# Performance work log

Hardware: AMD Instinct MI355X
Metric: run time of the kernel (lower is better)

The kernel has to match this reference:

```python
import jax, jax.numpy as jnp
import numpy as np

LN_EPS = 1e-5


def setup_inputs() -> dict:
    key = jax.random.key(0)
    ks = jax.random.split(key, 6)
    B, N, C, H = 8, 4096, 768, 12
    D = C // H
    x = jax.random.normal(ks[0], (B, N, C), dtype=jnp.float32)
    w_qkv = jax.random.normal(ks[1], (3 * C, C), dtype=jnp.float32) * (C ** -0.5)
    w_proj = jax.random.normal(ks[2], (C, C), dtype=jnp.float32) * (C ** -0.5)
    b_proj = jnp.zeros((C,), dtype=jnp.float32)
    # trunc_normal_(std=0.02) approximated by clipped normal
    p1 = jnp.clip(jax.random.normal(ks[3], (H, N), dtype=jnp.float32) * 0.02, -0.04, 0.04)
    p2 = jnp.clip(jax.random.normal(ks[4], (H, N), dtype=jnp.float32) * 0.02, -0.04, 0.04)
    gamma = jnp.ones((D,), dtype=jnp.float32)
    beta = jnp.zeros((D,), dtype=jnp.float32)
    return {"x": x, "w_qkv": w_qkv, "w_proj": w_proj, "b_proj": b_proj,
            "p1": p1, "p2": p2, "gamma": gamma, "beta": beta}


def _layernorm(h, gamma, beta):
    mu = jnp.mean(h, axis=-1, keepdims=True)
    var = jnp.var(h, axis=-1, keepdims=True)
    return (h - mu) * jax.lax.rsqrt(var + LN_EPS) * gamma + beta


def reference(x, w_qkv, w_proj, b_proj, p1, p2, gamma, beta):
    B, N, C = x.shape
    H = p1.shape[0]
    D = C // H
    # qkv projection (no bias): [B,N,3C] -> [3,B,H,N,D]
    qkv = (x @ w_qkv.T).reshape(B, N, 3, H, D).transpose(2, 0, 3, 1, 4)
    q, k, v = qkv[0], qkv[1], qkv[2]
    # weighted k*v reduction over sequence: [B,H,D]
    modulator = jnp.einsum('hn,bhnd->bhd', p2, k * v)
    modulator = _layernorm(modulator, gamma, beta)
    # broadcast modulation back over N: [B,H,N,D]
    modulator = jnp.einsum('hn,bhd->bhnd', p1, modulator)
    out = (q * modulator).transpose(0, 2, 1, 3).reshape(B, N, C)
    return out @ w_proj.T + b_proj
```

## Files before the change

kernel.cpp:

```cpp
#include <hip/hip_runtime.h>
#include <stdint.h>
#include <stddef.h>

#define LN_EPS 1e-5f

typedef __bf16 bf16;
typedef __bf16 bf16x8 __attribute__((ext_vector_type(8)));
typedef __bf16 bf16x4 __attribute__((ext_vector_type(4)));
typedef float f32x4 __attribute__((ext_vector_type(4)));

#define GL16(gp, lp)                                                                   \
  __builtin_amdgcn_global_load_lds((__attribute__((address_space(1))) uint32_t*)(gp),  \
                                   (__attribute__((address_space(3))) uint32_t*)(lp),  \
                                   16, 0, 0)

#define SBAR   asm volatile("s_barrier" ::: "memory")
#define LGK0   asm volatile("s_waitcnt lgkmcnt(0)" ::: "memory")
#define VMW(N) asm volatile("s_waitcnt vmcnt(" #N ")" ::: "memory")
#define NOWAIT ((void)0)

#define XV4   6291456
#define WQV4  442368
#define WPV4  147456
__global__ __launch_bounds__(256) void cvt_all(const float* __restrict__ x,
                                               const float* __restrict__ wq,
                                               const float* __restrict__ wp,
                                               bf16* __restrict__ xb,
                                               bf16* __restrict__ wqb,
                                               bf16* __restrict__ wpb) {
  int i = blockIdx.x * 256 + threadIdx.x;
  const float* src; bf16* dst; int off;
  if (i < XV4)              { src = x;  dst = xb;  off = i; }
  else if (i < XV4 + WQV4)  { src = wq; dst = wqb; off = i - XV4; }
  else                      { src = wp; dst = wpb; off = i - (XV4 + WQV4); }
  const float4 v = ((const float4*)src)[off];
  bf16x4 o;
  o[0] = (bf16)v.x; o[1] = (bf16)v.y; o[2] = (bf16)v.z; o[3] = (bf16)v.w;
  ((bf16x4*)dst)[off] = o;
}

#define STAGE_A(T, KH, SLOT) do {                      \
    GL16(pA0 + (T)*64 + (KH)*32, dA + (SLOT)*8192);    \
    GL16(pA1 + (T)*64 + (KH)*32, dA + (SLOT)*8192 + 4096); } while (0)

#define STAGE_B(T, KH, SLOT) do {                      \
    GL16(pB0 + (T)*64 + (KH)*32, dB + (SLOT)*8192);    \
    GL16(pB1 + (T)*64 + (KH)*32, dB + (SLOT)*8192 + 4096); } while (0)

#define PHASE(SLOT, MH, RB, STG, WAIT) do {                                         \
    if (RB) {                                                                       \
      _Pragma("unroll") for (int n = 0; n < 4; ++n)                                 \
        bF[n] = *(const bf16x8*)(ldsB + (SLOT)*8192 + (rB + n*16)*32 + colE);       \
    }                                                                               \
    _Pragma("unroll") for (int m = 0; m < 4; ++m)                                   \
      aF[m] = *(const bf16x8*)(ldsA + (SLOT)*8192 + (rA + (MH)*64 + m*16)*32 + colE); \
    STG;                                                                            \
    SBAR;                                                                           \
    LGK0;                                                                           \
    __builtin_amdgcn_sched_barrier(0);                                              \
    __builtin_amdgcn_s_setprio(1);                                                  \
    _Pragma("unroll") for (int m = 0; m < 4; ++m)                                   \
      _Pragma("unroll") for (int n = 0; n < 4; ++n)                                 \
        acc[(MH)*4 + m][n] =                                                        \
            __builtin_amdgcn_mfma_f32_16x16x32_bf16(aF[m], bF[n],                   \
                                                    acc[(MH)*4 + m][n], 0, 0, 0);   \
    __builtin_amdgcn_s_setprio(0);                                                  \
    WAIT;                                                                           \
    SBAR;                                                                           \
  } while (0)

#define TILE(SB, ST1, ST2, ST3, ST4, W2, W4) do { \
    PHASE((SB),     0, true,  ST1, NOWAIT);       \
    PHASE((SB),     1, false, ST2, W2);           \
    PHASE((SB) + 1, 0, true,  ST3, NOWAIT);       \
    PHASE((SB) + 1, 1, false, ST4, W4);           \
  } while (0)

__device__ __forceinline__ void gemm256(const bf16* pA0, const bf16* pA1,
                                        const bf16* pB0, const bf16* pB1,
                                        bf16* sh, f32x4 acc[8][4]) {
  const int tid  = threadIdx.x;
  const int lane = tid & 63;
  const int wave = tid >> 6;
  const int wm   = wave >> 2;
  const int wn   = wave & 3;
  const int l16  = lane & 15;
  const int colE = ((((lane >> 4) * 16) ^ (((l16 >> 1) & 3) << 4)) >> 1);
  bf16* const ldsA = sh;
  bf16* const ldsB = sh + 32768;
  bf16* const dA   = ldsA + tid * 8;
  bf16* const dB   = ldsB + tid * 8;
  const int rA = wm * 128 + l16;
  const int rB = wn * 64 + l16;
  bf16x8 aF[4], bF[4];

  STAGE_A(0, 0, 0); STAGE_B(0, 0, 0);
  STAGE_A(0, 1, 1); STAGE_B(0, 1, 1);
  STAGE_A(1, 0, 2); STAGE_B(1, 0, 2);
  VMW(8);
  SBAR;

  for (int T = 0; T < 10; T += 2) {
    TILE(0, STAGE_A(T+1,1,3), STAGE_B(T+1,1,3), STAGE_A(T+2,0,0), STAGE_B(T+2,0,0), VMW(8), VMW(8));
    TILE(2, STAGE_A(T+2,1,1), STAGE_B(T+2,1,1), STAGE_A(T+3,0,2), STAGE_B(T+3,0,2), VMW(8), VMW(8));
  }
  TILE(0, STAGE_A(11,1,3), STAGE_B(11,1,3), NOWAIT, NOWAIT, VMW(8), VMW(4));
  TILE(2, NOWAIT, NOWAIT, NOWAIT, NOWAIT, VMW(0), NOWAIT);

  asm volatile("s_waitcnt vmcnt(0) lgkmcnt(0)" ::: "memory");
  __syncthreads();
}

__global__ __launch_bounds__(512, 2) void kv_gemm_reduce(const bf16* __restrict__ A,
                                                         const bf16* __restrict__ B,
                                                         const float* __restrict__ p2,
                                                         float* __restrict__ partials) {
  __shared__ __align__(16) bf16 sh[65536];
  __shared__ float red[4][2][64];

  int lin = blockIdx.y * 6 + blockIdx.x;
  lin = (lin & 7) * 96 + (lin >> 3);
  const int hh   = lin % 6;
  const int mblk = lin / 6;
  const int m0   = mblk * 256;
  const int h0   = hh * 2;

  const int tid = threadIdx.x;
  const int rr  = tid >> 2;
  const int ck  = ((tid & 3) ^ ((tid >> 3) & 3)) * 8;
  const bf16* pA0 = A + (size_t)(m0 + rr) * 768 + ck;
  const bf16* pA1 = pA0 + (size_t)128 * 768;
  const int r1 = 128 + rr;
  const int wr0 = 768 + (((rr >> 6) & 1) * 768) + (h0 + (rr >> 7)) * 64 + (rr & 63);
  const int wr1 = 768 + (((r1 >> 6) & 1) * 768) + (h0 + (r1 >> 7)) * 64 + (r1 & 63);
  const bf16* pB0 = B + (size_t)wr0 * 768 + ck;
  const bf16* pB1 = B + (size_t)wr1 * 768 + ck;

  f32x4 acc[8][4] = {};
  gemm256(pA0, pA1, pB0, pB1, sh, acc);

  const int lane = tid & 63, wave = tid >> 6;
  const int wm = wave >> 2, wn = wave & 3, l16 = lane & 15;
  const int crow0 = wm * 128 + (lane >> 4) * 4;
  const int ccol0 = wn * 64 + l16;
#pragma unroll
  for (int mi = 0; mi < 8; ++mi)
#pragma unroll
    for (int ni = 0; ni < 4; ++ni)
#pragma unroll
      for (int r = 0; r < 4; ++r) {
        const int row = crow0 + mi * 16 + r;
        const int col = ccol0 + ni * 16;
        sh[row * 256 + (col ^ (((row >> 2) & 3) << 4))] = (bf16)acc[mi][ni][r];
      }
  __syncthreads();

  const int chunk = tid >> 7, hl = (tid >> 6) & 1, d = tid & 63;
  const float* pw = p2 + (size_t)(h0 + hl) * 4096 + (m0 & 4095) + chunk * 64;
  float s = 0.f;
#pragma unroll 8
  for (int n = 0; n < 64; ++n) {
    const int row = chunk * 64 + n;
    const int x = ((row >> 2) & 3) << 4;
    const float kk = (float)sh[row * 256 + ((hl * 128 + d) ^ x)];
    const float vv = (float)sh[row * 256 + ((hl * 128 + 64 + d) ^ x)];
    s += pw[n] * kk * vv;
  }
  red[chunk][hl][d] = s;
  __syncthreads();
  if (tid < 128) {
    const int hx = tid >> 6, dd = tid & 63;
    partials[((size_t)mblk * 12 + h0 + hx) * 64 + dd] =
        red[0][hx][dd] + red[1][hx][dd] + red[2][hx][dd] + red[3][hx][dd];
  }
}

__global__ __launch_bounds__(64) void mod_reduce_ln(const float* __restrict__ partials,
                                                    const float* __restrict__ gamma,
                                                    const float* __restrict__ beta,
                                                    float* __restrict__ mod) {
  const int h = blockIdx.x, b = blockIdx.y;
  const int d = threadIdx.x;

  const float* p = partials + ((size_t)(b * 16) * 12 + h) * 64 + d;
  float s = 0.f;
#pragma unroll
  for (int mb = 0; mb < 16; ++mb) s += p[(size_t)mb * 12 * 64];

  float sum = s, sumsq = s * s;
#pragma unroll
  for (int o = 32; o > 0; o >>= 1) {
    sum   += __shfl_xor(sum, o);
    sumsq += __shfl_xor(sumsq, o);
  }
  const float mu  = sum * (1.f / 64.f);
  const float var = sumsq * (1.f / 64.f) - mu * mu;
  const float r   = rsqrtf(var + LN_EPS);
  mod[(b * 12 + h) * 64 + d] = (s - mu) * r * gamma[d] + beta[d];
}

__global__ __launch_bounds__(512, 2) void q_gemm_mod(const bf16* __restrict__ A,
                                                     const bf16* __restrict__ B,
                                                     const float* __restrict__ p1,
                                                     const float* __restrict__ mod,
                                                     bf16* __restrict__ amod) {
  __shared__ __align__(16) bf16 sh[65536];

  int lin = blockIdx.y * 3 + blockIdx.x;
  lin = (lin & 7) * 48 + (lin >> 3);
  const int n0 = (lin % 3) * 256;
  const int m0 = (lin / 3) * 256;

  const int tid = threadIdx.x;
  const int rr  = tid >> 2;
  const int ck  = ((tid & 3) ^ ((tid >> 3) & 3)) * 8;
  const bf16* pA0 = A + (size_t)(m0 + rr) * 768 + ck;
  const bf16* pA1 = pA0 + (size_t)128 * 768;
  const bf16* pB0 = B + (size_t)(n0 + rr) * 768 + ck;
  const bf16* pB1 = pB0 + (size_t)128 * 768;

  f32x4 acc[8][4] = {};
  gemm256(pA0, pA1, pB0, pB1, sh, acc);

  const int lane = tid & 63, wave = tid >> 6;
  const int wm = wave >> 2, wn = wave & 3, l16 = lane & 15;
  const int row0 = m0 + wm * 128 + (lane >> 4) * 4;
  const int col0 = n0 + wn * 64 + l16;
  const int b    = m0 >> 12;
  const int h    = (n0 >> 6) + wn;

  float p1v[8][4];
#pragma unroll
  for (int mi = 0; mi < 8; ++mi)
#pragma unroll
    for (int r = 0; r < 4; ++r)
      p1v[mi][r] = p1[(size_t)h * 4096 + ((row0 + mi * 16 + r) & 4095)];
  float mv[4];
#pragma unroll
  for (int ni = 0; ni < 4; ++ni) mv[ni] = mod[b * 768 + col0 + ni * 16];

#pragma unroll
  for (int mi = 0; mi < 8; ++mi)
#pragma unroll
    for (int ni = 0; ni < 4; ++ni)
#pragma unroll
      for (int r = 0; r < 4; ++r)
        amod[(size_t)(row0 + mi * 16 + r) * 768 + col0 + ni * 16] =
            (bf16)(acc[mi][ni][r] * p1v[mi][r] * mv[ni]);
}

__global__ __launch_bounds__(512, 2) void gemm_proj(const bf16* __restrict__ A,
                                                    const bf16* __restrict__ B,
                                                    const float* __restrict__ bias,
                                                    float* __restrict__ C) {
  __shared__ __align__(16) bf16 sh[65536];

  int lin = blockIdx.y * 3 + blockIdx.x;
  lin = (lin & 7) * 48 + (lin >> 3);
  const int n0 = (lin % 3) * 256;
  const int m0 = (lin / 3) * 256;

  const int tid = threadIdx.x;
  const int rr  = tid >> 2;
  const int ck  = ((tid & 3) ^ ((tid >> 3) & 3)) * 8;
  const bf16* pA0 = A + (size_t)(m0 + rr) * 768 + ck;
  const bf16* pA1 = pA0 + (size_t)128 * 768;
  const bf16* pB0 = B + (size_t)(n0 + rr) * 768 + ck;
  const bf16* pB1 = pB0 + (size_t)128 * 768;

  f32x4 acc[8][4] = {};
  gemm256(pA0, pA1, pB0, pB1, sh, acc);

  const int lane = tid & 63, wave = tid >> 6;
  const int wm = wave >> 2, wn = wave & 3, l16 = lane & 15;
  const int row0 = m0 + wm * 128 + (lane >> 4) * 4;
  const int col0 = n0 + wn * 64 + l16;
#pragma unroll
  for (int ni = 0; ni < 4; ++ni) {
    const int col = col0 + ni * 16;
    const float bv = bias[col];
#pragma unroll
    for (int mi = 0; mi < 8; ++mi)
#pragma unroll
      for (int r = 0; r < 4; ++r)
        C[(size_t)(row0 + mi * 16 + r) * 768 + col] = acc[mi][ni][r] + bv;
  }
}

extern "C" void kernel_launch(void* const* d_in, const int* in_sizes, int n_in,
                              void* d_out, int out_size, void* d_ws, size_t ws_size,
                              hipStream_t stream) {
  (void)in_sizes; (void)n_in; (void)out_size; (void)ws_size;

  const float* x      = (const float*)d_in[0];
  const float* w_qkv  = (const float*)d_in[1];
  const float* w_proj = (const float*)d_in[2];
  const float* b_proj = (const float*)d_in[3];
  const float* p1     = (const float*)d_in[4];
  const float* p2     = (const float*)d_in[5];
  const float* gamma  = (const float*)d_in[6];
  const float* beta   = (const float*)d_in[7];
  float* out = (float*)d_out;

  char* ws = (char*)d_ws;
  bf16*  xb       = (bf16*)(ws + 0);
  bf16*  wqb      = (bf16*)(ws + 50331648);
  bf16*  wpb      = (bf16*)(ws + 53870592);
  bf16*  amod     = (bf16*)(ws + 55050240);
  float* partials = (float*)(ws + 105381888);
  float* mod      = (float*)(ws + 106168320);

  cvt_all<<<26880, 256, 0, stream>>>(x, w_qkv, w_proj, xb, wqb, wpb);

  kv_gemm_reduce<<<dim3(6, 128), 512, 0, stream>>>(xb, wqb, p2, partials);

  mod_reduce_ln<<<dim3(12, 8), 64, 0, stream>>>(partials, gamma, beta, mod);

  q_gemm_mod<<<dim3(3, 128), 512, 0, stream>>>(xb, wqb, p1, mod, amod);

  gemm_proj<<<dim3(3, 128), 512, 0, stream>>>(amod, wpb, b_proj, out);
}
```

Before: 379.5 us.

## Double-buffer LDS fragment reads across phases and transpose epilogue staging layout

Restructures the GEMM main loop so the A/B fragment reads for the next phase are issued before the MFMAs of the current phase. Two register sets of fragments alternate, and partial lgkmcnt waits replace the full wait, which removes one barrier per phase and overlaps LDS reads with matrix math. The k*v epilogue now writes accumulators transposed into a padded (264-wide) LDS tile with packed 4-element stores. The reduction then reads 8-element vectors along the sequence instead of scalar swizzled loads. This costs more registers and a slightly larger LDS footprint, which could hurt occupancy at 2 blocks per CU.

```diff
diff --git a/kernel.cpp b/kernel.cpp
--- a/kernel.cpp
+++ b/kernel.cpp
@@ -15,8 +15,8 @@
                                    16, 0, 0)
 
 #define SBAR   asm volatile("s_barrier" ::: "memory")
-#define LGK0   asm volatile("s_waitcnt lgkmcnt(0)" ::: "memory")
 #define VMW(N) asm volatile("s_waitcnt vmcnt(" #N ")" ::: "memory")
+#define LGK(N) asm volatile("s_waitcnt lgkmcnt(" #N ")" ::: "memory")
 #define NOWAIT ((void)0)
 
 #define XV4   6291456
@@ -39,41 +39,54 @@
   ((bf16x4*)dst)[off] = o;
 }
 
-#define STAGE_A(T, KH, SLOT) do {                      \
-    GL16(pA0 + (T)*64 + (KH)*32, dA + (SLOT)*8192);    \
-    GL16(pA1 + (T)*64 + (KH)*32, dA + (SLOT)*8192 + 4096); } while (0)
-
-#define STAGE_B(T, KH, SLOT) do {                      \
-    GL16(pB0 + (T)*64 + (KH)*32, dB + (SLOT)*8192);    \
-    GL16(pB1 + (T)*64 + (KH)*32, dB + (SLOT)*8192 + 4096); } while (0)
-
-#define PHASE(SLOT, MH, RB, STG, WAIT) do {                                         \
-    if (RB) {                                                                       \
-      _Pragma("unroll") for (int n = 0; n < 4; ++n)                                 \
-        bF[n] = *(const bf16x8*)(ldsB + (SLOT)*8192 + (rB + n*16)*32 + colE);       \
-    }                                                                               \
-    _Pragma("unroll") for (int m = 0; m < 4; ++m)                                   \
-      aF[m] = *(const bf16x8*)(ldsA + (SLOT)*8192 + (rA + (MH)*64 + m*16)*32 + colE); \
-    STG;                                                                            \
-    SBAR;                                                                           \
-    LGK0;                                                                           \
-    __builtin_amdgcn_sched_barrier(0);                                              \
-    __builtin_amdgcn_s_setprio(1);                                                  \
-    _Pragma("unroll") for (int m = 0; m < 4; ++m)                                   \
-      _Pragma("unroll") for (int n = 0; n < 4; ++n)                                 \
-        acc[(MH)*4 + m][n] =                                                        \
-            __builtin_amdgcn_mfma_f32_16x16x32_bf16(aF[m], bF[n],                   \
-                                                    acc[(MH)*4 + m][n], 0, 0, 0);   \
-    __builtin_amdgcn_s_setprio(0);                                                  \
-    WAIT;                                                                           \
-    SBAR;                                                                           \
+#define STAGE_A2(H, SL) do {                          \
+    GL16(pA0 + (H)*32, dA + (SL)*8192);               \
+    GL16(pA1 + (H)*32, dA + (SL)*8192 + 4096); } while (0)
+
+#define STAGE_B2(H, SL) do {                          \
+    GL16(pB0 + (H)*32, dB + (SL)*8192);               \
+    GL16(pB1 + (H)*32, dB + (SL)*8192 + 4096); } while (0)
+
+#define RD_B(DST, SL)                                                              \
+    _Pragma("unroll") for (int n = 0; n < 4; ++n)                                  \
+      DST[n] = *(const bf16x8*)(ldsB + (SL)*8192 + (rB + n*16)*32 + colE)
+
+#define RD_A0(DST, SL)                                                             \
+    _Pragma("unroll") for (int m = 0; m < 4; ++m)                                  \
+      DST[m] = *(const bf16x8*)(ldsA + (SL)*8192 + (rA + m*16)*32 + colE)
+
+#define RD_A1(SL)                                                                  \
+    _Pragma("unroll") for (int m = 0; m < 4; ++m)                                  \
+      af1[m] = *(const bf16x8*)(ldsA + (SL)*8192 + (rA + 64 + m*16)*32 + colE)
+
+#define MM(AF, BF, MO)                                                             \
+    _Pragma("unroll") for (int m = 0; m < 4; ++m)                                  \
+      _Pragma("unroll") for (int n = 0; n < 4; ++n)                                \
+        acc[(MO) + m][n] = __builtin_amdgcn_mfma_f32_16x16x32_bf16(                \
+            AF[m], BF[n], acc[(MO) + m][n], 0, 0, 0)
+
+#define EV_PHASE(SL, A0C, BFC, STG, WAITV) do {       \
+    RD_A1(SL);                                        \
+    STG;                                              \
+    LGK(4);                                           \
+    __builtin_amdgcn_sched_barrier(0);                \
+    __builtin_amdgcn_s_setprio(1);                    \
+    MM(A0C, BFC, 0);                                  \
+    __builtin_amdgcn_s_setprio(0);                    \
+    WAITV;                                            \
+    SBAR;                                             \
   } while (0)
 
-#define TILE(SB, ST1, ST2, ST3, ST4, W2, W4) do { \
-    PHASE((SB),     0, true,  ST1, NOWAIT);       \
-    PHASE((SB),     1, false, ST2, W2);           \
-    PHASE((SB) + 1, 0, true,  ST3, NOWAIT);       \
-    PHASE((SB) + 1, 1, false, ST4, W4);           \
+#define OD_PHASE(NSL, A0N, BFN, BFC, STG, LGKW) do {  \
+    RD_B(BFN, NSL);                                   \
+    RD_A0(A0N, NSL);                                  \
+    STG;                                              \
+    LGKW;                                             \
+    __builtin_amdgcn_sched_barrier(0);                \
+    __builtin_amdgcn_s_setprio(1);                    \
+    MM(af1, BFC, 4);                                  \
+    __builtin_amdgcn_s_setprio(0);                    \
+    SBAR;                                             \
   } while (0)
 
 __device__ __forceinline__ void gemm256(const bf16* pA0, const bf16* pA1,
@@ -92,21 +105,38 @@
   bf16* const dB   = ldsB + tid * 8;
   const int rA = wm * 128 + l16;
   const int rB = wn * 64 + l16;
-  bf16x8 aF[4], bF[4];
-
-  STAGE_A(0, 0, 0); STAGE_B(0, 0, 0);
-  STAGE_A(0, 1, 1); STAGE_B(0, 1, 1);
-  STAGE_A(1, 0, 2); STAGE_B(1, 0, 2);
+  bf16x8 af0X[4], af0Y[4], af1[4], bfX[4], bfY[4];
+
+  STAGE_A2(0, 0); STAGE_B2(0, 0);
+  STAGE_A2(1, 1); STAGE_B2(1, 1);
+  STAGE_A2(2, 2); STAGE_B2(2, 2);
   VMW(8);
   SBAR;
-
-  for (int T = 0; T < 10; T += 2) {
-    TILE(0, STAGE_A(T+1,1,3), STAGE_B(T+1,1,3), STAGE_A(T+2,0,0), STAGE_B(T+2,0,0), VMW(8), VMW(8));
-    TILE(2, STAGE_A(T+2,1,1), STAGE_B(T+2,1,1), STAGE_A(T+3,0,2), STAGE_B(T+3,0,2), VMW(8), VMW(8));
-  }
-  TILE(0, STAGE_A(11,1,3), STAGE_B(11,1,3), NOWAIT, NOWAIT, VMW(8), VMW(4));
-  TILE(2, NOWAIT, NOWAIT, NOWAIT, NOWAIT, VMW(0), NOWAIT);
-
+  RD_B(bfX, 0);
+  RD_A0(af0X, 0);
+
+  for (int h4 = 0; h4 < 20; h4 += 4) {
+    EV_PHASE(0, af0X, bfX, STAGE_A2(h4 + 3, 3), VMW(6));
+    OD_PHASE(1, af0Y, bfY, bfX, STAGE_B2(h4 + 3, 3), LGK(8));
+    EV_PHASE(1, af0Y, bfY, STAGE_A2(h4 + 4, 0), VMW(6));
+    OD_PHASE(2, af0X, bfX, bfY, STAGE_B2(h4 + 4, 0), LGK(8));
+    EV_PHASE(2, af0X, bfX, STAGE_A2(h4 + 5, 1), VMW(6));
+    OD_PHASE(3, af0Y, bfY, bfX, STAGE_B2(h4 + 5, 1), LGK(8));
+    EV_PHASE(3, af0Y, bfY, STAGE_A2(h4 + 6, 2), VMW(6));
+    OD_PHASE(0, af0X, bfX, bfY, STAGE_B2(h4 + 6, 2), LGK(8));
+  }
+  EV_PHASE(0, af0X, bfX, STAGE_A2(23, 3), VMW(6));
+  OD_PHASE(1, af0Y, bfY, bfX, STAGE_B2(23, 3), LGK(8));
+  EV_PHASE(1, af0Y, bfY, NOWAIT, VMW(4));
+  OD_PHASE(2, af0X, bfX, bfY, NOWAIT, LGK(8));
+  EV_PHASE(2, af0X, bfX, NOWAIT, VMW(0));
+  OD_PHASE(3, af0Y, bfY, bfX, NOWAIT, LGK(8));
+  EV_PHASE(3, af0Y, bfY, NOWAIT, NOWAIT);
+  LGK(0);
+  __builtin_amdgcn_sched_barrier(0);
+  __builtin_amdgcn_s_setprio(1);
+  MM(af1, bfY, 4);
+  __builtin_amdgcn_s_setprio(0);
   asm volatile("s_waitcnt vmcnt(0) lgkmcnt(0)" ::: "memory");
   __syncthreads();
 }
@@ -115,7 +145,7 @@
                                                          const bf16* __restrict__ B,
                                                          const float* __restrict__ p2,
                                                          float* __restrict__ partials) {
-  __shared__ __align__(16) bf16 sh[65536];
+  __shared__ __align__(16) bf16 sh[256 * 264];
   __shared__ float red[4][2][64];
 
   int lin = blockIdx.y * 6 + blockIdx.x;
@@ -141,32 +171,33 @@
 
   const int lane = tid & 63, wave = tid >> 6;
   const int wm = wave >> 2, wn = wave & 3, l16 = lane & 15;
-  const int crow0 = wm * 128 + (lane >> 4) * 4;
-  const int ccol0 = wn * 64 + l16;
-#pragma unroll
-  for (int mi = 0; mi < 8; ++mi)
-#pragma unroll
-    for (int ni = 0; ni < 4; ++ni)
-#pragma unroll
-      for (int r = 0; r < 4; ++r) {
-        const int row = crow0 + mi * 16 + r;
-        const int col = ccol0 + ni * 16;
-        sh[row * 256 + (col ^ (((row >> 2) & 3) << 4))] = (bf16)acc[mi][ni][r];
-      }
+  const int c0 = wn * 64 + l16;
+  const int r0 = wm * 128 + (lane >> 4) * 4;
+#pragma unroll
+  for (int ni = 0; ni < 4; ++ni)
+#pragma unroll
+    for (int mi = 0; mi < 8; ++mi) {
+      bf16x4 pk;
+      pk[0] = (bf16)acc[mi][ni][0]; pk[1] = (bf16)acc[mi][ni][1];
+      pk[2] = (bf16)acc[mi][ni][2]; pk[3] = (bf16)acc[mi][ni][3];
+      *(bf16x4*)(sh + (size_t)(c0 + ni * 16) * 264 + r0 + mi * 16) = pk;
+    }
   __syncthreads();
 
-  const int chunk = tid >> 7, hl = (tid >> 6) & 1, d = tid & 63;
-  const float* pw = p2 + (size_t)(h0 + hl) * 4096 + (m0 & 4095) + chunk * 64;
+  const int nq = tid >> 7, hl = (tid >> 6) & 1, d = tid & 63;
+  const float* pw = p2 + (size_t)(h0 + hl) * 4096 + (m0 & 4095) + nq * 64;
+  const bf16* pk = sh + (size_t)(hl * 128 + d) * 264 + nq * 64;
+  const bf16* pv = sh + (size_t)(hl * 128 + 64 + d) * 264 + nq * 64;
   float s = 0.f;
-#pragma unroll 8
-  for (int n = 0; n < 64; ++n) {
-    const int row = chunk * 64 + n;
-    const int x = ((row >> 2) & 3) << 4;
-    const float kk = (float)sh[row * 256 + ((hl * 128 + d) ^ x)];
-    const float vv = (float)sh[row * 256 + ((hl * 128 + 64 + d) ^ x)];
-    s += pw[n] * kk * vv;
-  }
-  red[chunk][hl][d] = s;
+#pragma unroll
+  for (int nb = 0; nb < 8; ++nb) {
+    const bf16x8 k8 = *(const bf16x8*)(pk + nb * 8);
+    const bf16x8 v8 = *(const bf16x8*)(pv + nb * 8);
+#pragma unroll
+    for (int e = 0; e < 8; ++e)
+      s += pw[nb * 8 + e] * (float)k8[e] * (float)v8[e];
+  }
+  red[nq][hl][d] = s;
   __syncthreads();
   if (tid < 128) {
     const int hx = tid >> 6, dd = tid & 63;
```

Measured after the change: 374.5 us. No clear change (-1.3%).

## Restructure bf16 GEMM mainloop with 64-wide K tiles and quarter-tile pipelining

Applied to the files above, without the earlier changes.

Reworks the shared GEMM core from 32-wide K half-tiles into full 64-wide K tiles split across four LDS quadrants. It adds a new XOR swizzle and an eight-step schedule that interleaves LDS fragment reads, async global-to-LDS staging and MFMA bursts with finer-grained waits. It also changes the XCD-aware block mapping and replaces the kv reduction's swizzled LDS scratch with a padded stride-260 layout read via float4 weights. The aim is better overlap of memory and matrix work and fewer bank conflicts, at the cost of more barriers and a riskier hand-tuned pipeline.

```diff
diff --git a/kernel.cpp b/kernel.cpp
--- a/kernel.cpp
+++ b/kernel.cpp
@@ -15,8 +15,11 @@
                                    16, 0, 0)
 
 #define SBAR   asm volatile("s_barrier" ::: "memory")
-#define LGK0   asm volatile("s_waitcnt lgkmcnt(0)" ::: "memory")
 #define VMW(N) asm volatile("s_waitcnt vmcnt(" #N ")" ::: "memory")
+#define LGK(N) asm volatile("s_waitcnt lgkmcnt(" #N ")" ::: "memory")
+#define SCB    __builtin_amdgcn_sched_barrier(0)
+#define SP1    __builtin_amdgcn_s_setprio(1)
+#define SP0    __builtin_amdgcn_s_setprio(0)
 #define NOWAIT ((void)0)
 
 #define XV4   6291456
@@ -39,75 +42,92 @@
   ((bf16x4*)dst)[off] = o;
 }
 
-#define STAGE_A(T, KH, SLOT) do {                      \
-    GL16(pA0 + (T)*64 + (KH)*32, dA + (SLOT)*8192);    \
-    GL16(pA1 + (T)*64 + (KH)*32, dA + (SLOT)*8192 + 4096); } while (0)
-
-#define STAGE_B(T, KH, SLOT) do {                      \
-    GL16(pB0 + (T)*64 + (KH)*32, dB + (SLOT)*8192);    \
-    GL16(pB1 + (T)*64 + (KH)*32, dB + (SLOT)*8192 + 4096); } while (0)
-
-#define PHASE(SLOT, MH, RB, STG, WAIT) do {                                         \
-    if (RB) {                                                                       \
-      _Pragma("unroll") for (int n = 0; n < 4; ++n)                                 \
-        bF[n] = *(const bf16x8*)(ldsB + (SLOT)*8192 + (rB + n*16)*32 + colE);       \
-    }                                                                               \
-    _Pragma("unroll") for (int m = 0; m < 4; ++m)                                   \
-      aF[m] = *(const bf16x8*)(ldsA + (SLOT)*8192 + (rA + (MH)*64 + m*16)*32 + colE); \
-    STG;                                                                            \
-    SBAR;                                                                           \
-    LGK0;                                                                           \
-    __builtin_amdgcn_sched_barrier(0);                                              \
-    __builtin_amdgcn_s_setprio(1);                                                  \
-    _Pragma("unroll") for (int m = 0; m < 4; ++m)                                   \
-      _Pragma("unroll") for (int n = 0; n < 4; ++n)                                 \
-        acc[(MH)*4 + m][n] =                                                        \
-            __builtin_amdgcn_mfma_f32_16x16x32_bf16(aF[m], bF[n],                   \
-                                                    acc[(MH)*4 + m][n], 0, 0, 0);   \
-    __builtin_amdgcn_s_setprio(0);                                                  \
-    WAIT;                                                                           \
-    SBAR;                                                                           \
+#define STAGE_A(T, H) do {                                              \
+    bf16* d_ = ldsA + ((((T)&1) << 1) + (H)) * 8192 + tid8;             \
+    GL16(pA + (H) * 98304 + (T) * 64, d_);                              \
+    GL16(pA + (H) * 98304 + 49152 + (T) * 64, d_ + 4096); } while (0)
+
+#define STAGE_B(T, H) do {                                              \
+    bf16* d_ = ldsB + ((((T)&1) << 1) + (H)) * 8192 + tid8;             \
+    GL16(pB##H##0 + (T) * 64, d_);                                      \
+    GL16(pB##H##1 + (T) * 64, d_ + 4096); } while (0)
+
+#define RD_AQ(D, MQ) do {                                               \
+    _Pragma("unroll") for (int mf = 0; mf < 4; ++mf) {                  \
+      const int r_ = (MQ) * 64 + mf * 16 + l16;                         \
+      const bf16* b_ = ldsA + (((D) << 1) + wm) * 8192 + r_ * 64;       \
+      const int x_ = r_ & 7;                                            \
+      aF[mf][0] = *(const bf16x8*)(b_ + ((qg ^ x_) << 3));              \
+      aF[mf][1] = *(const bf16x8*)(b_ + (((4 + qg) ^ x_) << 3));        \
+    } } while (0)
+
+#define RD_BQ(D, NQ, BF) do {                                           \
+    _Pragma("unroll") for (int nf = 0; nf < 2; ++nf) {                  \
+      const int r_ = hn64 + (NQ) * 32 + nf * 16 + l16;                  \
+      const bf16* b_ = ldsB + (((D) << 1) + hb) * 8192 + r_ * 64;       \
+      const int x_ = r_ & 7;                                            \
+      BF[nf][0] = *(const bf16x8*)(b_ + ((qg ^ x_) << 3));              \
+      BF[nf][1] = *(const bf16x8*)(b_ + (((4 + qg) ^ x_) << 3));        \
+    } } while (0)
+
+#define MMQ(MQ, NQ, BF) do {                                            \
+    _Pragma("unroll") for (int mf = 0; mf < 4; ++mf)                    \
+      _Pragma("unroll") for (int nf = 0; nf < 2; ++nf) {                \
+        acc[(MQ)*4+mf][(NQ)*2+nf] = __builtin_amdgcn_mfma_f32_16x16x32_bf16( \
+            aF[mf][0], BF[nf][0], acc[(MQ)*4+mf][(NQ)*2+nf], 0, 0, 0);  \
+        acc[(MQ)*4+mf][(NQ)*2+nf] = __builtin_amdgcn_mfma_f32_16x16x32_bf16( \
+            aF[mf][1], BF[nf][1], acc[(MQ)*4+mf][(NQ)*2+nf], 0, 0, 0);  \
+      } } while (0)
+
+#define ITER(T, P12, P38, WV4, WV8) do {                                       \
+     RD_AQ(0, 0); RD_BQ(0, 0, bF0); if (P12) STAGE_A((T)+1, 0); LGK(8);\
+    SBAR; LGK(0); SCB; SP1; MMQ(0, 0, bF0); SP0; SBAR;                         \
+     RD_BQ(0, 1, bF1); if (P12) STAGE_A((T)+1, 1);                     \
+    SBAR; LGK(0); SCB; SP1; MMQ(0, 1, bF1); SP0; SBAR;                         \
+     RD_AQ(0, 1); if (P38) STAGE_B((T)+2, 0);                          \
+    SBAR; LGK(0); SCB; SP1; MMQ(1, 0, bF0); SP0; SBAR;                         \
+     if (P38) STAGE_B((T)+2, 1);                                       \
+    SBAR; LGK(0); SCB; SP1; MMQ(1, 1, bF1); SP0; WV4; SBAR;                    \
+     RD_AQ(1, 0); RD_BQ(1, 0, bF0); if (P38) STAGE_A((T)+2, 0); LGK(8);\
+    SBAR; LGK(0); SCB; SP1; MMQ(0, 0, bF0); SP0; SBAR;                         \
+     RD_BQ(1, 1, bF1); if (P38) STAGE_A((T)+2, 1);                     \
+    SBAR; LGK(0); SCB; SP1; MMQ(0, 1, bF1); SP0; SBAR;                         \
+     RD_AQ(1, 1); if (P38) STAGE_B((T)+3, 0);                          \
+    SBAR; LGK(0); SCB; SP1; MMQ(1, 0, bF0); SP0; SBAR;                         \
+     if (P38) STAGE_B((T)+3, 1);                                       \
+    SBAR; LGK(0); SCB; SP1; MMQ(1, 1, bF1); SP0; WV8; SBAR;                    \
   } while (0)
 
-#define TILE(SB, ST1, ST2, ST3, ST4, W2, W4) do { \
-    PHASE((SB),     0, true,  ST1, NOWAIT);       \
-    PHASE((SB),     1, false, ST2, W2);           \
-    PHASE((SB) + 1, 0, true,  ST3, NOWAIT);       \
-    PHASE((SB) + 1, 1, false, ST4, W4);           \
-  } while (0)
-
-__device__ __forceinline__ void gemm256(const bf16* pA0, const bf16* pA1,
-                                        const bf16* pB0, const bf16* pB1,
+__device__ __forceinline__ void gemm256(const bf16* pA,
+                                        const bf16* pB00, const bf16* pB01,
+                                        const bf16* pB10, const bf16* pB11,
                                         bf16* sh, f32x4 acc[8][4]) {
   const int tid  = threadIdx.x;
   const int lane = tid & 63;
   const int wave = tid >> 6;
   const int wm   = wave >> 2;
   const int wn   = wave & 3;
+  const int hb   = wn >> 1;
+  const int hn64 = (wn & 1) * 64;
   const int l16  = lane & 15;
-  const int colE = ((((lane >> 4) * 16) ^ (((l16 >> 1) & 3) << 4)) >> 1);
+  const int qg   = lane >> 4;
+  const int tid8 = tid * 8;
   bf16* const ldsA = sh;
   bf16* const ldsB = sh + 32768;
-  bf16* const dA   = ldsA + tid * 8;
-  bf16* const dB   = ldsB + tid * 8;
-  const int rA = wm * 128 + l16;
-  const int rB = wn * 64 + l16;
-  bf16x8 aF[4], bF[4];
-
-  STAGE_A(0, 0, 0); STAGE_B(0, 0, 0);
-  STAGE_A(0, 1, 1); STAGE_B(0, 1, 1);
-  STAGE_A(1, 0, 2); STAGE_B(1, 0, 2);
+  bf16x8 aF[4][2], bF0[2][2], bF1[2][2];
+
+  STAGE_A(0, 0); STAGE_A(0, 1); STAGE_B(0, 0); STAGE_B(0, 1);
+  STAGE_A(1, 0); STAGE_A(1, 1); STAGE_B(1, 0); STAGE_B(1, 1);
   VMW(8);
   SBAR;
 
-  for (int T = 0; T < 10; T += 2) {
-    TILE(0, STAGE_A(T+1,1,3), STAGE_B(T+1,1,3), STAGE_A(T+2,0,0), STAGE_B(T+2,0,0), VMW(8), VMW(8));
-    TILE(2, STAGE_A(T+2,1,1), STAGE_B(T+2,1,1), STAGE_A(T+3,0,2), STAGE_B(T+3,0,2), VMW(8), VMW(8));
-  }
-  TILE(0, STAGE_A(11,1,3), STAGE_B(11,1,3), NOWAIT, NOWAIT, VMW(8), VMW(4));
-  TILE(2, NOWAIT, NOWAIT, NOWAIT, NOWAIT, VMW(0), NOWAIT);
-
-  asm volatile("s_waitcnt vmcnt(0) lgkmcnt(0)" ::: "memory");
+  ITER(0, 0, 1, VMW(4), VMW(4));
+#pragma unroll 1
+  for (int T = 2; T <= 8; T += 2) {
+    ITER(T, 1, 1, VMW(4), VMW(4));
+  }
+  ITER(10, 1, 0, VMW(0), NOWAIT);
+
   __syncthreads();
 }
 
@@ -115,58 +135,57 @@
                                                          const bf16* __restrict__ B,
                                                          const float* __restrict__ p2,
                                                          float* __restrict__ partials) {
-  __shared__ __align__(16) bf16 sh[65536];
+  __shared__ __align__(16) bf16 sh[66560];
   __shared__ float red[4][2][64];
 
-  int lin = blockIdx.y * 6 + blockIdx.x;
-  lin = (lin & 7) * 96 + (lin >> 3);
-  const int hh   = lin % 6;
-  const int mblk = lin / 6;
+  const int lin  = blockIdx.y * 6 + blockIdx.x;
+  const int xcd  = lin & 7;
+  const int j    = lin >> 3;
+  const int hh   = j % 6;
+  const int mblk = xcd + 8 * (j / 6);
   const int m0   = mblk * 256;
   const int h0   = hh * 2;
 
   const int tid = threadIdx.x;
-  const int rr  = tid >> 2;
-  const int ck  = ((tid & 3) ^ ((tid >> 3) & 3)) * 8;
-  const bf16* pA0 = A + (size_t)(m0 + rr) * 768 + ck;
-  const bf16* pA1 = pA0 + (size_t)128 * 768;
-  const int r1 = 128 + rr;
-  const int wr0 = 768 + (((rr >> 6) & 1) * 768) + (h0 + (rr >> 7)) * 64 + (rr & 63);
-  const int wr1 = 768 + (((r1 >> 6) & 1) * 768) + (h0 + (r1 >> 7)) * 64 + (r1 & 63);
-  const bf16* pB0 = B + (size_t)wr0 * 768 + ck;
-  const bf16* pB1 = B + (size_t)wr1 * 768 + ck;
+  const int tr  = tid >> 3;
+  const int tc  = ((tid & 7) ^ ((tid >> 3) & 7)) * 8;
+  const bf16* pA   = A + (size_t)(m0 + tr) * 768 + tc;
+  const bf16* pB00 = B + (size_t)(768  + (h0 + 0) * 64 + tr) * 768 + tc;
+  const bf16* pB01 = B + (size_t)(1536 + (h0 + 0) * 64 + tr) * 768 + tc;
+  const bf16* pB10 = B + (size_t)(768  + (h0 + 1) * 64 + tr) * 768 + tc;
+  const bf16* pB11 = B + (size_t)(1536 + (h0 + 1) * 64 + tr) * 768 + tc;
 
   f32x4 acc[8][4] = {};
-  gemm256(pA0, pA1, pB0, pB1, sh, acc);
+  gemm256(pA, pB00, pB01, pB10, pB11, sh, acc);
 
   const int lane = tid & 63, wave = tid >> 6;
-  const int wm = wave >> 2, wn = wave & 3, l16 = lane & 15;
-  const int crow0 = wm * 128 + (lane >> 4) * 4;
-  const int ccol0 = wn * 64 + l16;
+  const int wm = wave >> 2, wn = wave & 3, l16 = lane & 15, qg = lane >> 4;
+  const int r0s = wm * 128 + qg * 4;
+  const int c0s = wn * 64 + l16;
 #pragma unroll
   for (int mi = 0; mi < 8; ++mi)
 #pragma unroll
     for (int ni = 0; ni < 4; ++ni)
 #pragma unroll
-      for (int r = 0; r < 4; ++r) {
-        const int row = crow0 + mi * 16 + r;
-        const int col = ccol0 + ni * 16;
-        sh[row * 256 + (col ^ (((row >> 2) & 3) << 4))] = (bf16)acc[mi][ni][r];
-      }
+      for (int r = 0; r < 4; ++r)
+        sh[(size_t)(r0s + mi * 16 + r) * 260 + c0s + ni * 16] = (bf16)acc[mi][ni][r];
   __syncthreads();
 
-  const int chunk = tid >> 7, hl = (tid >> 6) & 1, d = tid & 63;
-  const float* pw = p2 + (size_t)(h0 + hl) * 4096 + (m0 & 4095) + chunk * 64;
+  const int nq = tid >> 7, hl = (tid >> 6) & 1, d = tid & 63;
+  const float4* pw4 = (const float4*)(p2 + (size_t)(h0 + hl) * 4096 + (m0 & 4095) + nq * 64);
+  const bf16* pk = sh + (size_t)(nq * 64) * 260 + hl * 128 + d;
+  const bf16* pv = pk + 64;
   float s = 0.f;
-#pragma unroll 8
-  for (int n = 0; n < 64; ++n) {
-    const int row = chunk * 64 + n;
-    const int x = ((row >> 2) & 3) << 4;
-    const float kk = (float)sh[row * 256 + ((hl * 128 + d) ^ x)];
-    const float vv = (float)sh[row * 256 + ((hl * 128 + 64 + d) ^ x)];
-    s += pw[n] * kk * vv;
-  }
-  red[chunk][hl][d] = s;
+#pragma unroll
+  for (int nb = 0; nb < 16; ++nb) {
+    const float4 w = pw4[nb];
+    const int n = nb * 4;
+    s += w.x * (float)pk[(n + 0) * 260] * (float)pv[(n + 0) * 260]
+       + w.y * (float)pk[(n + 1) * 260] * (float)pv[(n + 1) * 260]
+       + w.z * (float)pk[(n + 2) * 260] * (float)pv[(n + 2) * 260]
+       + w.w * (float)pk[(n + 3) * 260] * (float)pv[(n + 3) * 260];
+  }
+  red[nq][hl][d] = s;
   __syncthreads();
   if (tid < 128) {
     const int hx = tid >> 6, dd = tid & 63;
@@ -206,21 +225,25 @@
                                                      bf16* __restrict__ amod) {
   __shared__ __align__(16) bf16 sh[65536];
 
-  int lin = blockIdx.y * 3 + blockIdx.x;
-  lin = (lin & 7) * 48 + (lin >> 3);
-  const int n0 = (lin % 3) * 256;
-  const int m0 = (lin / 3) * 256;
+  const int lin  = blockIdx.y * 3 + blockIdx.x;
+  const int xcd  = lin & 7;
+  const int j    = lin >> 3;
+  const int nblk = j % 3;
+  const int mblk = xcd + 8 * (j / 3);
+  const int n0   = nblk * 256;
+  const int m0   = mblk * 256;
 
   const int tid = threadIdx.x;
-  const int rr  = tid >> 2;
-  const int ck  = ((tid & 3) ^ ((tid >> 3) & 3)) * 8;
-  const bf16* pA0 = A + (size_t)(m0 + rr) * 768 + ck;
-  const bf16* pA1 = pA0 + (size_t)128 * 768;
-  const bf16* pB0 = B + (size_t)(n0 + rr) * 768 + ck;
-  const bf16* pB1 = pB0 + (size_t)128 * 768;
+  const int tr  = tid >> 3;
+  const int tc  = ((tid & 7) ^ ((tid >> 3) & 7)) * 8;
+  const bf16* pA   = A + (size_t)(m0 + tr) * 768 + tc;
+  const bf16* pB00 = B + (size_t)(n0 + tr) * 768 + tc;
+  const bf16* pB01 = pB00 + (size_t)64 * 768;
+  const bf16* pB10 = pB00 + (size_t)128 * 768;
+  const bf16* pB11 = pB00 + (size_t)192 * 768;
 
   f32x4 acc[8][4] = {};
-  gemm256(pA0, pA1, pB0, pB1, sh, acc);
+  gemm256(pA, pB00, pB01, pB10, pB11, sh, acc);
 
   const int lane = tid & 63, wave = tid >> 6;
   const int wm = wave >> 2, wn = wave & 3, l16 = lane & 15;
@@ -255,21 +278,25 @@
                                                     float* __restrict__ C) {
   __shared__ __align__(16) bf16 sh[65536];
 
-  int lin = blockIdx.y * 3 + blockIdx.x;
-  lin = (lin & 7) * 48 + (lin >> 3);
-  const int n0 = (lin % 3) * 256;
-  const int m0 = (lin / 3) * 256;
+  const int lin  = blockIdx.y * 3 + blockIdx.x;
+  const int xcd  = lin & 7;
+  const int j    = lin >> 3;
+  const int nblk = j % 3;
+  const int mblk = xcd + 8 * (j / 3);
+  const int n0   = nblk * 256;
+  const int m0   = mblk * 256;
 
   const int tid = threadIdx.x;
-  const int rr  = tid >> 2;
-  const int ck  = ((tid & 3) ^ ((tid >> 3) & 3)) * 8;
-  const bf16* pA0 = A + (size_t)(m0 + rr) * 768 + ck;
-  const bf16* pA1 = pA0 + (size_t)128 * 768;
-  const bf16* pB0 = B + (size_t)(n0 + rr) * 768 + ck;
-  const bf16* pB1 = pB0 + (size_t)128 * 768;
+  const int tr  = tid >> 3;
+  const int tc  = ((tid & 7) ^ ((tid >> 3) & 7)) * 8;
+  const bf16* pA   = A + (size_t)(m0 + tr) * 768 + tc;
+  const bf16* pB00 = B + (size_t)(n0 + tr) * 768 + tc;
+  const bf16* pB01 = pB00 + (size_t)64 * 768;
+  const bf16* pB10 = pB00 + (size_t)128 * 768;
+  const bf16* pB11 = pB00 + (size_t)192 * 768;
 
   f32x4 acc[8][4] = {};
-  gemm256(pA0, pA1, pB0, pB1, sh, acc);
+  gemm256(pA, pB00, pB01, pB10, pB11, sh, acc);
 
   const int lane = tid & 63, wave = tid >> 6;
   const int wm = wave >> 2, wn = wave & 3, l16 = lane & 15;
```

After: 372.8 us. No clear change (-1.8%).
